# Kernel optimization log

Measured on AMD Instinct MI355X. Metric: run time of the kernel, lower is better.

## Reference

```python
import jax, jax.numpy as jnp
import numpy as np

N_LABELS = 301   # vessel labels 1..301; label 0 is background
N_GROUPS = 7     # stands in for RandInt(1, n_groups=10)() in the original
VOL = (256, 256, 256)


def setup_inputs() -> dict:
    key = jax.random.key(0)
    k1, k2, k3 = jax.random.split(key, 3)
    # integer vessel-ID volume (0 = background)
    vessel_labels = jax.random.randint(k1, VOL, 0, N_LABELS + 1, dtype=jnp.int32)
    # stand-ins for the cornucopia random-field transforms (parenchyma_ outputs)
    parenchyma = jax.random.uniform(k2, VOL, jnp.float32, 0.5, 2.0)
    vessel_texture = jax.random.uniform(k3, VOL, jnp.float32, 0.8, 1.2)
    # label -> intensity LUT replicating the grouped masked_fill loop:
    # sorted labels split into N_GROUPS consecutive chunks, each chunk sharing
    # one Uniform(0.25, 0.75) intensity; background (label 0) stays 0.
    per_group = int(np.ceil(N_LABELS / N_GROUPS))
    group_intensity = np.random.RandomState(0).uniform(0.25, 0.75, N_GROUPS).astype(np.float32)
    lut = np.repeat(group_intensity, per_group)[:N_LABELS]
    intensity_lut = jnp.concatenate([jnp.zeros((1,), jnp.float32), jnp.asarray(lut)])
    return {
        "vessel_labels": vessel_labels,
        "parenchyma": parenchyma,
        "vessel_texture": vessel_texture,
        "intensity_lut": intensity_lut,
    }


def reference(vessel_labels, parenchyma, vessel_texture, intensity_lut):
    # vessels_: the per-label masked_fill_ loop collapses into one gather
    scaling = intensity_lut[vessel_labels]          # [X,Y,Z] float32
    vessels = scaling * vessel_texture              # intensity * texture
    vessels = jnp.where(vessels == 0.0, jnp.float32(1.0), vessels)  # vessels[vessels==0]=1
    final_volume = parenchyma * vessels
    vessel_mask = vessel_labels.astype(bool)
    return final_volume, vessel_mask
```

## Files before the change

### kernel.cpp

```cpp
#include <hip/hip_runtime.h>


#define N_ELEMS (256 * 256 * 256)
#define LUT_SIZE 302
#define BLOCK 512
#define CHUNKS 2

typedef float vfloat4 __attribute__((ext_vector_type(4)));
typedef int   vint4   __attribute__((ext_vector_type(4)));

#define GLOAD(dst, off, base, imm)                                    \
  asm volatile("global_load_dwordx4 %0, %1, %2 offset:" #imm          \
               : "=&v"(dst) : "v"(off), "s"(base))

#define GSTORE_NT(src, off, base, imm)                                \
  asm volatile("global_store_dwordx4 %0, %1, %2 offset:" #imm " nt"   \
               :: "v"(off), "v"(src), "s"(base) : "memory")

#define WAITCNT_VM(n)                                                 \
  do {                                                                \
    asm volatile("s_waitcnt vmcnt(" #n ")" ::: "memory");             \
    __builtin_amdgcn_sched_barrier(0);                                \
  } while (0)

__global__ __launch_bounds__(BLOCK) void octvolsynth_r8(
    const int* __restrict__ labels,
    const float* __restrict__ parenchyma,
    const float* __restrict__ texture,
    const float* __restrict__ lut,
    float* __restrict__ out)
{
    __shared__ float s_lut[LUT_SIZE];
    for (int i = threadIdx.x; i < LUT_SIZE; i += BLOCK) s_lut[i] = lut[i];
    __syncthreads();

    const unsigned wid  = threadIdx.x >> 6;
    const unsigned lane = threadIdx.x & 63;
    const unsigned off = blockIdx.x * (BLOCK * CHUNKS * 16u)
                       + wid * (CHUNKS * 64u * 16u)
                       + lane * 16u;

    const float* outm = out + N_ELEMS;

    vint4   l0, l1;
    vfloat4 p0, p1, x0, x1;
    GLOAD(l0, off, labels,     0);
    GLOAD(p0, off, parenchyma, 0);
    GLOAD(x0, off, texture,    0);
    GLOAD(l1, off, labels,     1024);
    GLOAD(p1, off, parenchyma, 1024);
    GLOAD(x1, off, texture,    1024);

#define DO_CHUNK(L, P, X, imm) do {                                   \
    float v0 = s_lut[(L).x] * (X).x;                                  \
    float v1 = s_lut[(L).y] * (X).y;                                  \
    float v2 = s_lut[(L).z] * (X).z;                                  \
    float v3 = s_lut[(L).w] * (X).w;                                  \
    vfloat4 fv, mv;                                                   \
    fv.x = (P).x * ((v0 == 0.0f) ? 1.0f : v0);                        \
    fv.y = (P).y * ((v1 == 0.0f) ? 1.0f : v1);                        \
    fv.z = (P).z * ((v2 == 0.0f) ? 1.0f : v2);                        \
    fv.w = (P).w * ((v3 == 0.0f) ? 1.0f : v3);                        \
    mv.x = ((L).x != 0) ? 1.0f : 0.0f;                                \
    mv.y = ((L).y != 0) ? 1.0f : 0.0f;                                \
    mv.z = ((L).z != 0) ? 1.0f : 0.0f;                                \
    mv.w = ((L).w != 0) ? 1.0f : 0.0f;                                \
    GSTORE_NT(fv, off, out,  imm);                                    \
    GSTORE_NT(mv, off, outm, imm);                                    \
} while (0)

    WAITCNT_VM(3);
    DO_CHUNK(l0, p0, x0, 0);
    WAITCNT_VM(2);
    DO_CHUNK(l1, p1, x1, 1024);

#undef DO_CHUNK
}

extern "C" void kernel_launch(void* const* d_in, const int* in_sizes, int n_in,
                              void* d_out, int out_size, void* d_ws, size_t ws_size,
                              hipStream_t stream) {
    const int*   labels     = (const int*)d_in[0];
    const float* parenchyma = (const float*)d_in[1];
    const float* texture    = (const float*)d_in[2];
    const float* lut        = (const float*)d_in[3];
    float* out = (float*)d_out;

    const int grid = (N_ELEMS * 4) / (BLOCK * CHUNKS * 16);
    octvolsynth_r8<<<grid, BLOCK, 0, stream>>>(labels, parenchyma, texture, lut, out);
}
```

Before: 281.6 us.

## Software-pipeline eight tiles per block with triple-buffered loads over a fixed grid

Each block now covers eight contiguous 8 KB tiles instead of two interleaved chunks, and the grid is fixed at 1024 blocks. The kernel keeps three register sets of label, parenchyma and texture vectors in flight and uses explicit vmcnt waits, so loads for later tiles overlap with compute and stores for earlier ones. This also spreads the per-block LUT staging and barrier over more work. Stores lose the non-temporal hint, and the extra register sets plus the launch-bounds occupancy hint may reduce how many waves run at once.

```diff
diff --git a/kernel.cpp b/kernel.cpp
--- a/kernel.cpp
+++ b/kernel.cpp
@@ -4,26 +4,26 @@
 #define N_ELEMS (256 * 256 * 256)
 #define LUT_SIZE 302
 #define BLOCK 512
-#define CHUNKS 2
+#define GRID 1024
+#define TILE_BYTES 8192
+#define BLK_BYTES (8 * TILE_BYTES)
 
 typedef float vfloat4 __attribute__((ext_vector_type(4)));
 typedef int   vint4   __attribute__((ext_vector_type(4)));
 
-#define GLOAD(dst, off, base, imm)                                    \
-  asm volatile("global_load_dwordx4 %0, %1, %2 offset:" #imm          \
+#define GLOAD(dst, off, base)                                         \
+  asm volatile("global_load_dwordx4 %0, %1, %2"                       \
                : "=&v"(dst) : "v"(off), "s"(base))
 
-#define GSTORE_NT(src, off, base, imm)                                \
-  asm volatile("global_store_dwordx4 %0, %1, %2 offset:" #imm " nt"   \
+#define GSTORE(src, off, base)                                        \
+  asm volatile("global_store_dwordx4 %0, %1, %2"                      \
                :: "v"(off), "v"(src), "s"(base) : "memory")
 
-#define WAITCNT_VM(n)                                                 \
-  do {                                                                \
-    asm volatile("s_waitcnt vmcnt(" #n ")" ::: "memory");             \
-    __builtin_amdgcn_sched_barrier(0);                                \
-  } while (0)
+#define WAITSB(n)                                                     \
+  do { asm volatile("s_waitcnt vmcnt(" #n ")" ::: "memory");          \
+       __builtin_amdgcn_sched_barrier(0); } while (0)
 
-__global__ __launch_bounds__(BLOCK) void octvolsynth_r8(
+__global__ __launch_bounds__(BLOCK, 8) void octvolsynth_r9(
     const int* __restrict__ labels,
     const float* __restrict__ parenchyma,
     const float* __restrict__ texture,
@@ -34,24 +34,19 @@
     for (int i = threadIdx.x; i < LUT_SIZE; i += BLOCK) s_lut[i] = lut[i];
     __syncthreads();
 
-    const unsigned wid  = threadIdx.x >> 6;
-    const unsigned lane = threadIdx.x & 63;
-    const unsigned off = blockIdx.x * (BLOCK * CHUNKS * 16u)
-                       + wid * (CHUNKS * 64u * 16u)
-                       + lane * 16u;
-
+    const unsigned o0 = blockIdx.x * (unsigned)BLK_BYTES + threadIdx.x * 16u;
     const float* outm = out + N_ELEMS;
 
-    vint4   l0, l1;
-    vfloat4 p0, p1, x0, x1;
-    GLOAD(l0, off, labels,     0);
-    GLOAD(p0, off, parenchyma, 0);
-    GLOAD(x0, off, texture,    0);
-    GLOAD(l1, off, labels,     1024);
-    GLOAD(p1, off, parenchyma, 1024);
-    GLOAD(x1, off, texture,    1024);
+    vint4   lA, lB, lC;
+    vfloat4 pA, pB, pC, xA, xB, xC;
 
-#define DO_CHUNK(L, P, X, imm) do {                                   \
+#define ISSUE(L, P, X, off) do {                                      \
+    GLOAD(L, (off), labels);                                          \
+    GLOAD(P, (off), parenchyma);                                      \
+    GLOAD(X, (off), texture);                                         \
+} while (0)
+
+#define CONSUME(L, P, X, off) do {                                    \
     float v0 = s_lut[(L).x] * (X).x;                                  \
     float v1 = s_lut[(L).y] * (X).y;                                  \
     float v2 = s_lut[(L).z] * (X).z;                                  \
@@ -65,16 +60,36 @@
     mv.y = ((L).y != 0) ? 1.0f : 0.0f;                                \
     mv.z = ((L).z != 0) ? 1.0f : 0.0f;                                \
     mv.w = ((L).w != 0) ? 1.0f : 0.0f;                                \
-    GSTORE_NT(fv, off, out,  imm);                                    \
-    GSTORE_NT(mv, off, outm, imm);                                    \
+    GSTORE(fv, (off), out);                                           \
+    GSTORE(mv, (off), outm);                                          \
 } while (0)
 
-    WAITCNT_VM(3);
-    DO_CHUNK(l0, p0, x0, 0);
-    WAITCNT_VM(2);
-    DO_CHUNK(l1, p1, x1, 1024);
+    ISSUE(lA, pA, xA, o0 + 0 * TILE_BYTES);
+    ISSUE(lB, pB, xB, o0 + 1 * TILE_BYTES);
 
-#undef DO_CHUNK
+    ISSUE(lC, pC, xC, o0 + 2 * TILE_BYTES);
+    WAITSB(6);  CONSUME(lA, pA, xA, o0 + 0 * TILE_BYTES);
+
+    ISSUE(lA, pA, xA, o0 + 3 * TILE_BYTES);
+    WAITSB(8);  CONSUME(lB, pB, xB, o0 + 1 * TILE_BYTES);
+
+    ISSUE(lB, pB, xB, o0 + 4 * TILE_BYTES);
+    WAITSB(8);  CONSUME(lC, pC, xC, o0 + 2 * TILE_BYTES);
+
+    ISSUE(lC, pC, xC, o0 + 5 * TILE_BYTES);
+    WAITSB(8);  CONSUME(lA, pA, xA, o0 + 3 * TILE_BYTES);
+
+    ISSUE(lA, pA, xA, o0 + 6 * TILE_BYTES);
+    WAITSB(8);  CONSUME(lB, pB, xB, o0 + 4 * TILE_BYTES);
+
+    ISSUE(lB, pB, xB, o0 + 7 * TILE_BYTES);
+    WAITSB(8);  CONSUME(lC, pC, xC, o0 + 5 * TILE_BYTES);
+
+    WAITSB(7);  CONSUME(lA, pA, xA, o0 + 6 * TILE_BYTES);
+    WAITSB(4);  CONSUME(lB, pB, xB, o0 + 7 * TILE_BYTES);
+
+#undef ISSUE
+#undef CONSUME
 }
 
 extern "C" void kernel_launch(void* const* d_in, const int* in_sizes, int n_in,
@@ -86,6 +101,5 @@
     const float* lut        = (const float*)d_in[3];
     float* out = (float*)d_out;
 
-    const int grid = (N_ELEMS * 4) / (BLOCK * CHUNKS * 16);
-    octvolsynth_r8<<<grid, BLOCK, 0, stream>>>(labels, parenchyma, texture, lut, out);
+    octvolsynth_r9<<<GRID, BLOCK, 0, stream>>>(labels, parenchyma, texture, lut, out);
 }
```

Measured after the change: 276.4 us. No clear change (-1.8%).
